# Kernel optimization log

Hardware: AMD Instinct MI355X
Metric: run time of the kernel (lower is better)

The kernel has to match this reference:

```python
import jax, jax.numpy as jnp
import numpy as np

B, N, F_IN, F_OUT = 4, 4096, 128, 128

def setup_inputs() -> dict:
    key = jax.random.key(0)
    k1, k2, k3 = jax.random.split(key, 3)
    x = jax.random.normal(k1, (B, N, F_IN), dtype=jnp.float32)
    adj = jax.random.uniform(k2, (B, N, N), dtype=jnp.float32)
    weight = jax.random.normal(k3, (F_IN, F_OUT), dtype=jnp.float32) * (6.0 / (F_IN + F_OUT)) ** 0.5
    bias = jnp.zeros((F_OUT,), dtype=jnp.float32)
    return {"x": x, "adj": adj, "weight": weight, "bias": bias}

def reference(x, adj, weight, bias):
    # Z = D^{-1/2} A D^{-1/2} X W + b   (activation=None)
    degree = jnp.sum(adj, axis=-1)                       # [B, N]
    d_inv = jnp.power(degree + 1e-6, -0.5)               # [B, N]
    # diag(d_inv) @ A @ diag(d_inv) == row/col elementwise scaling
    adj_norm = d_inv[:, :, None] * adj * d_inv[:, None, :]  # [B, N, N]
    z = jnp.einsum('bnm,bmf->bnf', adj_norm, x)          # [B, N, F_in]
    z = jnp.einsum('bnf,fo->bno', z, weight) + bias      # [B, N, F_out]
    return z
```

## Files before the change

### kernel.cpp

```cpp
#include <hip/hip_runtime.h>
#include <hip/hip_bf16.h>
#include <stdint.h>


#define NROW 4096
#define FDIM 128
#define NBATCH 4

typedef __bf16 bf16x8 __attribute__((ext_vector_type(8)));
typedef float f32x4 __attribute__((ext_vector_type(4)));

__global__ __launch_bounds__(256) void k_degree(const float* __restrict__ adj,
                                                float* __restrict__ dinv) {
  const int row = blockIdx.x;
  const float4* arow = (const float4*)(adj + (size_t)row * NROW);
  const int tid = threadIdx.x;
  float s = 0.f;
#pragma unroll
  for (int i = 0; i < 4; ++i) {
    float4 v = arow[tid + i * 256];
    s += (v.x + v.y) + (v.z + v.w);
  }
#pragma unroll
  for (int off = 32; off > 0; off >>= 1) s += __shfl_down(s, off, 64);
  __shared__ float ps[4];
  if ((tid & 63) == 0) ps[tid >> 6] = s;
  __syncthreads();
  if (tid == 0) {
    float d = (ps[0] + ps[1]) + (ps[2] + ps[3]);
    dinv[row] = 1.0f / sqrtf(d + 1e-6f);
  }
}

__global__ __launch_bounds__(256) void k_xst(const float* __restrict__ x,
                                             const float* __restrict__ dinv,
                                             __hip_bfloat16* __restrict__ xst) {
  const int bid = blockIdx.x;
  const int b = bid >> 7;
  const int m0 = (bid & 127) * 32;
  const int tid = threadIdx.x;
  __shared__ float tile[32 * 132];

  {
    const int ml = tid >> 3;
    const int fl = (tid & 7) * 16;
    const float dv = dinv[b * NROW + m0 + ml];
    const float* gx = x + ((size_t)b * NROW + m0 + ml) * FDIM + fl;
    float* dst = &tile[ml * 132 + fl];
#pragma unroll
    for (int j = 0; j < 16; j += 4) {
      float4 v = *(const float4*)(gx + j);
      v.x *= dv; v.y *= dv; v.z *= dv; v.w *= dv;
      *(float4*)(dst + j) = v;
    }
  }
  __syncthreads();
  {
    const int f = tid >> 1;
    const int mc = (tid & 1) * 16;
    union { __hip_bfloat16 h[16]; uint4 v[2]; } tmp;
#pragma unroll
    for (int j = 0; j < 16; ++j)
      tmp.h[j] = __float2bfloat16(tile[(mc + j) * 132 + f]);
    __hip_bfloat16* dst = xst + ((size_t)b * FDIM + f) * NROW + m0 + mc;
    *(uint4*)(dst) = tmp.v[0];
    *(uint4*)(dst + 8) = tmp.v[1];
  }
}

#define MT 32
#define KC 64
#define AS_ST 72
#define BS_ST 72
#define ZS_ST 136
#define WT_ST 136

__global__ __launch_bounds__(256, 2)
void k_gemm(const float* __restrict__ adj, const __hip_bfloat16* __restrict__ xst,
            const float* __restrict__ dinv, const float* __restrict__ w,
            const float* __restrict__ bias, float* __restrict__ out) {
  __shared__ union {
    struct { __hip_bfloat16 As[MT * AS_ST]; __hip_bfloat16 Bs[FDIM * BS_ST]; } lp;
    struct { __hip_bfloat16 Zs[MT * ZS_ST]; __hip_bfloat16 Wt[FDIM * WT_ST]; } ep;
  } sm;
  __shared__ float dinv_s[MT];

  const int bid = blockIdx.x;
  const int xcd = bid & 7;
  const int b = xcd >> 1;
  const int mtile = (bid >> 3) * 2 + (xcd & 1);
  const int row0 = mtile * MT;

  const int tid = threadIdx.x;
  const int lane = tid & 63;
  const int wid = tid >> 6;
  const int l16 = lane & 15;
  const int quad = lane >> 4;

  if (tid < MT) dinv_s[tid] = dinv[b * NROW + row0 + tid];

  const float* adj_b = adj + ((size_t)b * NROW + row0) * NROW;
  const __hip_bfloat16* xst_b = xst + (size_t)b * FDIM * NROW;

  f32x4 zero4;
  zero4.x = 0.f; zero4.y = 0.f; zero4.z = 0.f; zero4.w = 0.f;
  f32x4 acc[2][2];
#pragma unroll
  for (int rt = 0; rt < 2; ++rt)
#pragma unroll
    for (int ct = 0; ct < 2; ++ct) acc[rt][ct] = zero4;

  const int ar = tid >> 3;
  const int ac = (tid & 7) * 8;
  const int bfr = tid >> 1;
  const int bcc = (tid & 1) * 32;
  const float* ga = adj_b + (size_t)ar * NROW + ac;
  const __hip_bfloat16* gb = xst_b + (size_t)bfr * NROW + bcc;

  for (int k0 = 0; k0 < NROW; k0 += KC) {
    {
      float4 v0 = *(const float4*)(ga + k0);
      float4 v1 = *(const float4*)(ga + k0 + 4);
      union { __hip_bfloat16 h[8]; uint4 u; } t;
      t.h[0] = __float2bfloat16(v0.x); t.h[1] = __float2bfloat16(v0.y);
      t.h[2] = __float2bfloat16(v0.z); t.h[3] = __float2bfloat16(v0.w);
      t.h[4] = __float2bfloat16(v1.x); t.h[5] = __float2bfloat16(v1.y);
      t.h[6] = __float2bfloat16(v1.z); t.h[7] = __float2bfloat16(v1.w);
      *(uint4*)&sm.lp.As[ar * AS_ST + ac] = t.u;
    }
    {
      const __hip_bfloat16* p = gb + k0;
      uint4 u0 = *(const uint4*)(p);
      uint4 u1 = *(const uint4*)(p + 8);
      uint4 u2 = *(const uint4*)(p + 16);
      uint4 u3 = *(const uint4*)(p + 24);
      __hip_bfloat16* q = &sm.lp.Bs[bfr * BS_ST + bcc];
      *(uint4*)(q) = u0;
      *(uint4*)(q + 8) = u1;
      *(uint4*)(q + 16) = u2;
      *(uint4*)(q + 24) = u3;
    }
    __syncthreads();
#pragma unroll
    for (int kk = 0; kk < 2; ++kk) {
      bf16x8 af[2], bfv[2];
#pragma unroll
      for (int rt = 0; rt < 2; ++rt)
        af[rt] = *(const bf16x8*)&sm.lp.As[(rt * 16 + l16) * AS_ST + kk * 32 + quad * 8];
#pragma unroll
      for (int ct = 0; ct < 2; ++ct)
        bfv[ct] = *(const bf16x8*)&sm.lp.Bs[(wid * 32 + ct * 16 + l16) * BS_ST + kk * 32 + quad * 8];
#pragma unroll
      for (int rt = 0; rt < 2; ++rt)
#pragma unroll
        for (int ct = 0; ct < 2; ++ct)
          acc[rt][ct] = __builtin_amdgcn_mfma_f32_16x16x32_bf16(af[rt], bfv[ct], acc[rt][ct], 0, 0, 0);
    }
    __syncthreads();
  }

#pragma unroll
  for (int rt = 0; rt < 2; ++rt)
#pragma unroll
    for (int ct = 0; ct < 2; ++ct)
#pragma unroll
      for (int i = 0; i < 4; ++i) {
        int r = rt * 16 + quad * 4 + i;
        int c = wid * 32 + ct * 16 + l16;
        sm.ep.Zs[r * ZS_ST + c] = __float2bfloat16(acc[rt][ct][i] * dinv_s[r]);
      }
  {
    const int f = tid >> 1;
    const int oc = (tid & 1) * 64;
    const float* gw = w + f * FDIM + oc;
#pragma unroll 4
    for (int j = 0; j < 64; j += 4) {
      float4 v = *(const float4*)(gw + j);
      sm.ep.Wt[(oc + j + 0) * WT_ST + f] = __float2bfloat16(v.x);
      sm.ep.Wt[(oc + j + 1) * WT_ST + f] = __float2bfloat16(v.y);
      sm.ep.Wt[(oc + j + 2) * WT_ST + f] = __float2bfloat16(v.z);
      sm.ep.Wt[(oc + j + 3) * WT_ST + f] = __float2bfloat16(v.w);
    }
  }
  __syncthreads();

  f32x4 acc2[2][2];
#pragma unroll
  for (int rt = 0; rt < 2; ++rt)
#pragma unroll
    for (int ct = 0; ct < 2; ++ct) acc2[rt][ct] = zero4;
#pragma unroll
  for (int kk = 0; kk < 4; ++kk) {
    bf16x8 za[2], wb[2];
#pragma unroll
    for (int rt = 0; rt < 2; ++rt)
      za[rt] = *(const bf16x8*)&sm.ep.Zs[(rt * 16 + l16) * ZS_ST + kk * 32 + quad * 8];
#pragma unroll
    for (int ct = 0; ct < 2; ++ct)
      wb[ct] = *(const bf16x8*)&sm.ep.Wt[(wid * 32 + ct * 16 + l16) * WT_ST + kk * 32 + quad * 8];
#pragma unroll
    for (int rt = 0; rt < 2; ++rt)
#pragma unroll
      for (int ct = 0; ct < 2; ++ct)
        acc2[rt][ct] = __builtin_amdgcn_mfma_f32_16x16x32_bf16(za[rt], wb[ct], acc2[rt][ct], 0, 0, 0);
  }

  float bv[2];
  bv[0] = bias[wid * 32 + l16];
  bv[1] = bias[wid * 32 + 16 + l16];
  float* ob = out + ((size_t)b * NROW + row0) * FDIM;
#pragma unroll
  for (int rt = 0; rt < 2; ++rt)
#pragma unroll
    for (int ct = 0; ct < 2; ++ct)
#pragma unroll
      for (int i = 0; i < 4; ++i) {
        int r = rt * 16 + quad * 4 + i;
        int o = wid * 32 + ct * 16 + l16;
        ob[(size_t)r * FDIM + o] = acc2[rt][ct][i] + bv[ct];
      }
}

extern "C" void kernel_launch(void* const* d_in, const int* in_sizes, int n_in,
                              void* d_out, int out_size, void* d_ws, size_t ws_size,
                              hipStream_t stream) {
  const float* x    = (const float*)d_in[0];
  const float* adj  = (const float*)d_in[1];
  const float* w    = (const float*)d_in[2];
  const float* bias = (const float*)d_in[3];
  float* out = (float*)d_out;

  float* dinv = (float*)d_ws;
  __hip_bfloat16* xst =
      (__hip_bfloat16*)((char*)d_ws + (size_t)NBATCH * NROW * sizeof(float));

  k_degree<<<NBATCH * NROW, 256, 0, stream>>>(adj, dinv);
  k_xst<<<512, 256, 0, stream>>>(x, dinv, xst);
  k_gemm<<<512, 256, 0, stream>>>(adj, xst, dinv, w, bias, out);
}
```

Before: 436.3 us.

## Double-buffer GEMM LDS with register prefetch, wave-per-row degree, direct W loads

The main GEMM loop now keeps two LDS buffers and prefetches the next adj/xst chunk into registers while computing the current one, which drops one barrier per iteration. The degree kernel assigns one wave per row, so block-level shared-memory reduction and its barrier go away. The epilogue reads W straight from global memory into MFMA fragments instead of staging a transposed copy in LDS. Doubling the LDS footprint raises per-block LDS use and may lower occupancy, and the strided W loads are uncoalesced.

```diff
diff --git a/kernel.cpp b/kernel.cpp
--- a/kernel.cpp
+++ b/kernel.cpp
@@ -12,24 +12,18 @@
 
 __global__ __launch_bounds__(256) void k_degree(const float* __restrict__ adj,
                                                 float* __restrict__ dinv) {
-  const int row = blockIdx.x;
+  const int row = blockIdx.x * 4 + (threadIdx.x >> 6);
+  const int lane = threadIdx.x & 63;
   const float4* arow = (const float4*)(adj + (size_t)row * NROW);
-  const int tid = threadIdx.x;
   float s = 0.f;
 #pragma unroll
-  for (int i = 0; i < 4; ++i) {
-    float4 v = arow[tid + i * 256];
+  for (int i = 0; i < 16; ++i) {
+    float4 v = arow[lane + i * 64];
     s += (v.x + v.y) + (v.z + v.w);
   }
 #pragma unroll
   for (int off = 32; off > 0; off >>= 1) s += __shfl_down(s, off, 64);
-  __shared__ float ps[4];
-  if ((tid & 63) == 0) ps[tid >> 6] = s;
-  __syncthreads();
-  if (tid == 0) {
-    float d = (ps[0] + ps[1]) + (ps[2] + ps[3]);
-    dinv[row] = 1.0f / sqrtf(d + 1e-6f);
-  }
+  if (lane == 0) dinv[row] = 1.0f / sqrtf(s + 1e-6f);
 }
 
 __global__ __launch_bounds__(256) void k_xst(const float* __restrict__ x,
@@ -73,15 +67,14 @@
 #define AS_ST 72
 #define BS_ST 72
 #define ZS_ST 136
-#define WT_ST 136
 
 __global__ __launch_bounds__(256, 2)
 void k_gemm(const float* __restrict__ adj, const __hip_bfloat16* __restrict__ xst,
             const float* __restrict__ dinv, const float* __restrict__ w,
             const float* __restrict__ bias, float* __restrict__ out) {
   __shared__ union {
-    struct { __hip_bfloat16 As[MT * AS_ST]; __hip_bfloat16 Bs[FDIM * BS_ST]; } lp;
-    struct { __hip_bfloat16 Zs[MT * ZS_ST]; __hip_bfloat16 Wt[FDIM * WT_ST]; } ep;
+    struct { __hip_bfloat16 As[2][MT * AS_ST]; __hip_bfloat16 Bs[2][FDIM * BS_ST]; } lp;
+    __hip_bfloat16 Zs[MT * ZS_ST];
   } sm;
   __shared__ float dinv_s[MT];
 
@@ -117,28 +110,37 @@
   const float* ga = adj_b + (size_t)ar * NROW + ac;
   const __hip_bfloat16* gb = xst_b + (size_t)bfr * NROW + bcc;
 
+  float4 pa0 = *(const float4*)(ga);
+  float4 pa1 = *(const float4*)(ga + 4);
+  uint4 pb0 = ((const uint4*)gb)[0];
+  uint4 pb1 = ((const uint4*)gb)[1];
+  uint4 pb2 = ((const uint4*)gb)[2];
+  uint4 pb3 = ((const uint4*)gb)[3];
+
+  int p = 0;
   for (int k0 = 0; k0 < NROW; k0 += KC) {
     {
-      float4 v0 = *(const float4*)(ga + k0);
-      float4 v1 = *(const float4*)(ga + k0 + 4);
       union { __hip_bfloat16 h[8]; uint4 u; } t;
-      t.h[0] = __float2bfloat16(v0.x); t.h[1] = __float2bfloat16(v0.y);
-      t.h[2] = __float2bfloat16(v0.z); t.h[3] = __float2bfloat16(v0.w);
-      t.h[4] = __float2bfloat16(v1.x); t.h[5] = __float2bfloat16(v1.y);
-      t.h[6] = __float2bfloat16(v1.z); t.h[7] = __float2bfloat16(v1.w);
-      *(uint4*)&sm.lp.As[ar * AS_ST + ac] = t.u;
-    }
-    {
-      const __hip_bfloat16* p = gb + k0;
-      uint4 u0 = *(const uint4*)(p);
-      uint4 u1 = *(const uint4*)(p + 8);
-      uint4 u2 = *(const uint4*)(p + 16);
-      uint4 u3 = *(const uint4*)(p + 24);
-      __hip_bfloat16* q = &sm.lp.Bs[bfr * BS_ST + bcc];
-      *(uint4*)(q) = u0;
-      *(uint4*)(q + 8) = u1;
-      *(uint4*)(q + 16) = u2;
-      *(uint4*)(q + 24) = u3;
+      t.h[0] = __float2bfloat16(pa0.x); t.h[1] = __float2bfloat16(pa0.y);
+      t.h[2] = __float2bfloat16(pa0.z); t.h[3] = __float2bfloat16(pa0.w);
+      t.h[4] = __float2bfloat16(pa1.x); t.h[5] = __float2bfloat16(pa1.y);
+      t.h[6] = __float2bfloat16(pa1.z); t.h[7] = __float2bfloat16(pa1.w);
+      *(uint4*)&sm.lp.As[p][ar * AS_ST + ac] = t.u;
+      __hip_bfloat16* q = &sm.lp.Bs[p][bfr * BS_ST + bcc];
+      *(uint4*)(q) = pb0;
+      *(uint4*)(q + 8) = pb1;
+      *(uint4*)(q + 16) = pb2;
+      *(uint4*)(q + 24) = pb3;
+    }
+    if (k0 + KC < NROW) {
+      const float* gan = ga + k0 + KC;
+      pa0 = *(const float4*)(gan);
+      pa1 = *(const float4*)(gan + 4);
+      const __hip_bfloat16* gbn = gb + k0 + KC;
+      pb0 = ((const uint4*)gbn)[0];
+      pb1 = ((const uint4*)gbn)[1];
+      pb2 = ((const uint4*)gbn)[2];
+      pb3 = ((const uint4*)gbn)[3];
     }
     __syncthreads();
 #pragma unroll
@@ -146,18 +148,19 @@
       bf16x8 af[2], bfv[2];
 #pragma unroll
       for (int rt = 0; rt < 2; ++rt)
-        af[rt] = *(const bf16x8*)&sm.lp.As[(rt * 16 + l16) * AS_ST + kk * 32 + quad * 8];
+        af[rt] = *(const bf16x8*)&sm.lp.As[p][(rt * 16 + l16) * AS_ST + kk * 32 + quad * 8];
 #pragma unroll
       for (int ct = 0; ct < 2; ++ct)
-        bfv[ct] = *(const bf16x8*)&sm.lp.Bs[(wid * 32 + ct * 16 + l16) * BS_ST + kk * 32 + quad * 8];
+        bfv[ct] = *(const bf16x8*)&sm.lp.Bs[p][(wid * 32 + ct * 16 + l16) * BS_ST + kk * 32 + quad * 8];
 #pragma unroll
       for (int rt = 0; rt < 2; ++rt)
 #pragma unroll
         for (int ct = 0; ct < 2; ++ct)
           acc[rt][ct] = __builtin_amdgcn_mfma_f32_16x16x32_bf16(af[rt], bfv[ct], acc[rt][ct], 0, 0, 0);
     }
-    __syncthreads();
-  }
+    p ^= 1;
+  }
+  __syncthreads();
 
 #pragma unroll
   for (int rt = 0; rt < 2; ++rt)
@@ -167,21 +170,8 @@
       for (int i = 0; i < 4; ++i) {
         int r = rt * 16 + quad * 4 + i;
         int c = wid * 32 + ct * 16 + l16;
-        sm.ep.Zs[r * ZS_ST + c] = __float2bfloat16(acc[rt][ct][i] * dinv_s[r]);
+        sm.Zs[r * ZS_ST + c] = __float2bfloat16(acc[rt][ct][i] * dinv_s[r]);
       }
-  {
-    const int f = tid >> 1;
-    const int oc = (tid & 1) * 64;
-    const float* gw = w + f * FDIM + oc;
-#pragma unroll 4
-    for (int j = 0; j < 64; j += 4) {
-      float4 v = *(const float4*)(gw + j);
-      sm.ep.Wt[(oc + j + 0) * WT_ST + f] = __float2bfloat16(v.x);
-      sm.ep.Wt[(oc + j + 1) * WT_ST + f] = __float2bfloat16(v.y);
-      sm.ep.Wt[(oc + j + 2) * WT_ST + f] = __float2bfloat16(v.z);
-      sm.ep.Wt[(oc + j + 3) * WT_ST + f] = __float2bfloat16(v.w);
-    }
-  }
   __syncthreads();
 
   f32x4 acc2[2][2];
@@ -194,10 +184,17 @@
     bf16x8 za[2], wb[2];
 #pragma unroll
     for (int rt = 0; rt < 2; ++rt)
-      za[rt] = *(const bf16x8*)&sm.ep.Zs[(rt * 16 + l16) * ZS_ST + kk * 32 + quad * 8];
-#pragma unroll
-    for (int ct = 0; ct < 2; ++ct)
-      wb[ct] = *(const bf16x8*)&sm.ep.Wt[(wid * 32 + ct * 16 + l16) * WT_ST + kk * 32 + quad * 8];
+      za[rt] = *(const bf16x8*)&sm.Zs[(rt * 16 + l16) * ZS_ST + kk * 32 + quad * 8];
+#pragma unroll
+    for (int ct = 0; ct < 2; ++ct) {
+      const int o = wid * 32 + ct * 16 + l16;
+      const float* gw = w + (kk * 32 + quad * 8) * FDIM + o;
+      union { __hip_bfloat16 h[8]; bf16x8 v; } tw;
+#pragma unroll
+      for (int j = 0; j < 8; ++j)
+        tw.h[j] = __float2bfloat16(gw[j * FDIM]);
+      wb[ct] = tw.v;
+    }
 #pragma unroll
     for (int rt = 0; rt < 2; ++rt)
 #pragma unroll
@@ -234,7 +231,7 @@
   __hip_bfloat16* xst =
       (__hip_bfloat16*)((char*)d_ws + (size_t)NBATCH * NROW * sizeof(float));
 
-  k_degree<<<NBATCH * NROW, 256, 0, stream>>>(adj, dinv);
+  k_degree<<<NBATCH * NROW / 4, 256, 0, stream>>>(adj, dinv);
   k_xst<<<512, 256, 0, stream>>>(x, dinv, xst);
   k_gemm<<<512, 256, 0, stream>>>(adj, xst, dinv, w, bias, out);
 }
```

Result: faster. 419.8 us (-3.8%).
